# Kernel tuning notes

Measured on AMD Instinct MI355X. Metric: run time of the kernel, lower is better.

## Reference

```python
import jax, jax.numpy as jnp
import numpy as np

B, L, N, S, M = 4096, 512, 12, 128, 12


def setup_inputs() -> dict:
    key = jax.random.key(0)
    ks = jax.random.split(key, 8)
    sc = 1.0 / np.sqrt(S)
    scn = 1.0 / np.sqrt(N)
    return {
        "x": jax.random.normal(ks[0], (B, L, N), dtype=jnp.float32),
        "a0": jax.random.uniform(ks[1], (B, S), dtype=jnp.float32),
        "U_w": jax.random.uniform(ks[2], (N, S), minval=-scn, maxval=scn, dtype=jnp.float32),
        "U_b": jax.random.uniform(ks[3], (S,), minval=-scn, maxval=scn, dtype=jnp.float32),
        "W_w": jax.random.uniform(ks[4], (S, S), minval=-sc, maxval=sc, dtype=jnp.float32),
        "W_b": jax.random.uniform(ks[5], (S,), minval=-sc, maxval=sc, dtype=jnp.float32),
        "V_w": jax.random.uniform(ks[6], (S, M), minval=-sc, maxval=sc, dtype=jnp.float32),
        "V_b": jax.random.uniform(ks[7], (M,), minval=-sc, maxval=sc, dtype=jnp.float32),
    }


def reference(x, a0, U_w, U_b, W_w, W_b, V_w, V_b):
    # Elman RNN cell: a_t = relu(U(x_t) + W(a_{t-1})); output y = V(a_L)
    # Precompute input projection for all steps at once: [B,L,S]
    ux = jnp.einsum("bln,ns->bls", x, U_w) + U_b

    def step(a, ux_t):  # a: [B,S], ux_t: [B,S]
        a_new = jax.nn.relu(ux_t + a @ W_w + W_b)
        return a_new, None

    a_last, _ = jax.lax.scan(step, a0, jnp.swapaxes(ux, 0, 1))  # scan over L
    return a_last @ V_w + V_b  # [B, M]
```

## Files before the change

### kernel.cpp

```cpp
#include <hip/hip_runtime.h>
#include <hip/hip_bf16.h>

typedef __attribute__((ext_vector_type(8))) short bf16x8;
typedef __attribute__((ext_vector_type(4))) float f32x4;

#define L_SEQ 512
#define N_IN 12
#define S_DIM 128
#define M_OUT 12
#define LPAD 40
#define KT_STRIDE (16*LPAD)

__device__ inline short f2bf(float f) {
    union { float f; unsigned u; } q; q.f = f;
    unsigned r = (q.u + 0x7fffu + ((q.u >> 16) & 1u)) >> 16;
    return (short)r;
}
__device__ inline unsigned cvtpk(float lo, float hi) {
    unsigned r;
    asm("v_cvt_pk_bf16_f32 %0, %1, %2" : "=v"(r) : "v"(lo), "v"(hi));
    return r;
}
__device__ inline int s_perm(int kt, int q, int j) {
    return 32 * kt + 16 * (j >> 2) + 4 * q + (j & 3);
}
__device__ inline void block_sync() {
    asm volatile("s_waitcnt lgkmcnt(0)" ::: "memory");
    __builtin_amdgcn_s_barrier();
}

__global__ __launch_bounds__(256, 1)
void elman_kernel(const float* __restrict__ x,
                  const float* __restrict__ a0,
                  const float* __restrict__ U_w,
                  const float* __restrict__ U_b,
                  const float* __restrict__ W_w,
                  const float* __restrict__ W_b,
                  const float* __restrict__ V_w,
                  const float* __restrict__ V_b,
                  float* __restrict__ out)
{
    __shared__ __align__(16) short stx[2][4 * KT_STRIDE];

    const int tid  = threadIdx.x;
    const int w    = tid >> 6;
    const int l    = tid & 63;
    const int n    = l & 15;
    const int q    = l >> 4;
    const bool qodd = (q & 1);
    const int b0   = blockIdx.x * 16;
    const int row  = b0 + n;

    bf16x8 wf[2][4]; bf16x8 uf[2];
    #pragma unroll
    for (int h = 0; h < 2; ++h) {
        const int c = (2 * w + h) * 16 + n;
        #pragma unroll
        for (int li = 0; li < 4; ++li) {
            const int kt = (w + li) & 3;
            #pragma unroll
            for (int j = 0; j < 8; ++j)
                wf[h][li][j] = f2bf(W_w[(size_t)s_perm(kt, q, j) * S_DIM + c]);
        }
        #pragma unroll
        for (int j = 0; j < 8; ++j) {
            const int k = q * 8 + j;
            float v;
            if (k < N_IN)       v = U_w[(size_t)k * S_DIM + c];
            else if (k == N_IN) v = W_b[c] + U_b[c];
            else                v = 0.f;
            uf[h][j] = f2bf(v);
        }
    }

    for (int idx = tid; idx < 4 * 16 * 32; idx += 256) {
        const int kt = idx >> 9, r = (idx >> 5) & 15, qj = idx & 31;
        const int s = s_perm(kt, qj >> 3, qj & 7);
        stx[0][kt * KT_STRIDE + r * LPAD + qj] = f2bf(a0[(size_t)(b0 + r) * S_DIM + s]);
    }
    block_sync();

    const int fragoff = n * LPAD + q * 8;
    bf16x8 stOwn = *(const bf16x8*)&stx[0][((w + 0) & 3) * KT_STRIDE + fragoff];
    bf16x8 stf1  = *(const bf16x8*)&stx[0][((w + 1) & 3) * KT_STRIDE + fragoff];
    bf16x8 stf2  = *(const bf16x8*)&stx[0][((w + 2) & 3) * KT_STRIDE + fragoff];
    bf16x8 stf3  = *(const bf16x8*)&stx[0][((w + 3) & 3) * KT_STRIDE + fragoff];

    const float* xpA = x + (size_t)row * L_SEQ * N_IN + (q & 1) * 8;
    const float* xpB = xpA + (qodd ? 0 : 4);
    float4 xa0 = *(const float4*)(xpA + 0 * N_IN), xb0 = *(const float4*)(xpB + 0 * N_IN);
    float4 xa1 = *(const float4*)(xpA + 1 * N_IN), xb1 = *(const float4*)(xpB + 1 * N_IN);
    float4 xa2 = *(const float4*)(xpA + 2 * N_IN), xb2 = *(const float4*)(xpB + 2 * N_IN);
    float4 xa3 = *(const float4*)(xpA + 3 * N_IN), xb3 = *(const float4*)(xpB + 3 * N_IN);

#define MAKE_XF(XF, XA, XB) do {                                                       \
    union { unsigned u[4]; bf16x8 v; } xu_;                                            \
    xu_.u[0] = cvtpk(XA.x, XA.y);                                                      \
    xu_.u[1] = cvtpk(XA.z, XA.w);                                                      \
    xu_.u[2] = qodd ? 0x00003F80u : cvtpk(XB.x, XB.y);         \
    xu_.u[3] = qodd ? 0u          : cvtpk(XB.z, XB.w);                                 \
    XF = xu_.v;                                                                        \
} while (0)

    f32x4 accU0, accU1;
    {
        bf16x8 xf; MAKE_XF(xf, xa0, xb0);
        f32x4 z = {0.f, 0.f, 0.f, 0.f};
        accU0 = __builtin_amdgcn_mfma_f32_16x16x32_bf16(uf[0], xf, z, 0, 0, 0);
        accU1 = __builtin_amdgcn_mfma_f32_16x16x32_bf16(uf[1], xf, z, 0, 0, 0);
        xa0 = *(const float4*)(xpA + 4 * N_IN);
        xb0 = *(const float4*)(xpB + 4 * N_IN);
    }

#define STEP(XA, XB, TT, TNEXT) do {                                                   \
    f32x4 acc0, acc1;                                                                  \
    acc0 = __builtin_amdgcn_mfma_f32_16x16x32_bf16(wf[0][0], stOwn, accU0, 0, 0, 0);   \
    acc1 = __builtin_amdgcn_mfma_f32_16x16x32_bf16(wf[1][0], stOwn, accU1, 0, 0, 0);   \
    acc0 = __builtin_amdgcn_mfma_f32_16x16x32_bf16(wf[0][1], stf1, acc0, 0, 0, 0);     \
    acc1 = __builtin_amdgcn_mfma_f32_16x16x32_bf16(wf[1][1], stf1, acc1, 0, 0, 0);     \
    acc0 = __builtin_amdgcn_mfma_f32_16x16x32_bf16(wf[0][2], stf2, acc0, 0, 0, 0);     \
    acc1 = __builtin_amdgcn_mfma_f32_16x16x32_bf16(wf[1][2], stf2, acc1, 0, 0, 0);     \
    acc0 = __builtin_amdgcn_mfma_f32_16x16x32_bf16(wf[0][3], stf3, acc0, 0, 0, 0);     \
    acc1 = __builtin_amdgcn_mfma_f32_16x16x32_bf16(wf[1][3], stf3, acc1, 0, 0, 0);     \
                                  \
    {                                                                                  \
        bf16x8 xf_; MAKE_XF(xf_, XA, XB);                                              \
        const int tl_ = ((TNEXT) < L_SEQ) ? (TNEXT) : (L_SEQ - 1);                     \
        XA = *(const float4*)(xpA + (size_t)tl_ * N_IN);                               \
        XB = *(const float4*)(xpB + (size_t)tl_ * N_IN);                               \
        f32x4 z_ = {0.f, 0.f, 0.f, 0.f};                                               \
        accU0 = __builtin_amdgcn_mfma_f32_16x16x32_bf16(uf[0], xf_, z_, 0, 0, 0);      \
        accU1 = __builtin_amdgcn_mfma_f32_16x16x32_bf16(uf[1], xf_, z_, 0, 0, 0);      \
    }                                                                                  \
                   \
    {                                                                                  \
        union { unsigned u[4]; bf16x8 v; } su_;                                        \
        su_.u[0] = cvtpk(fmaxf(acc0[0], 0.f), fmaxf(acc0[1], 0.f));                    \
        su_.u[1] = cvtpk(fmaxf(acc0[2], 0.f), fmaxf(acc0[3], 0.f));                    \
        su_.u[2] = cvtpk(fmaxf(acc1[0], 0.f), fmaxf(acc1[1], 0.f));                    \
        su_.u[3] = cvtpk(fmaxf(acc1[2], 0.f), fmaxf(acc1[3], 0.f));                    \
        stOwn = su_.v;                                                                 \
    }                                                                                  \
    short* wr_ = &stx[(TT + 1) & 1][w * KT_STRIDE + fragoff];                          \
    *(bf16x8*)wr_ = stOwn;                                                             \
    block_sync();                                                                      \
    const short* rd_ = &stx[(TT + 1) & 1][0];                                          \
    stf1 = *(const bf16x8*)&rd_[((w + 1) & 3) * KT_STRIDE + fragoff];                  \
    stf2 = *(const bf16x8*)&rd_[((w + 2) & 3) * KT_STRIDE + fragoff];                  \
    stf3 = *(const bf16x8*)&rd_[((w + 3) & 3) * KT_STRIDE + fragoff];                  \
} while (0)

    for (int t = 0; t < L_SEQ; t += 4) {
        STEP(xa1, xb1, t + 0, t + 5);
        STEP(xa2, xb2, t + 1, t + 6);
        STEP(xa3, xb3, t + 2, t + 7);
        STEP(xa0, xb0, t + 3, t + 8);
    }
#undef STEP
#undef MAKE_XF

    if (w == 0) {
        f32x4 acc = {0.f, 0.f, 0.f, 0.f};
        #pragma unroll
        for (int li = 0; li < 4; ++li) {
            bf16x8 vf;
            #pragma unroll
            for (int j = 0; j < 8; ++j)
                vf[j] = (n < M_OUT)
                      ? f2bf(V_w[(size_t)s_perm(li, q, j) * M_OUT + n])
                      : (short)0;
            const bf16x8 stt = (li == 0) ? stOwn : (li == 1) ? stf1 : (li == 2) ? stf2 : stf3;
            acc = __builtin_amdgcn_mfma_f32_16x16x32_bf16(vf, stt, acc, 0, 0, 0);
        }
        #pragma unroll
        for (int j = 0; j < 4; ++j) {
            const int m = 4 * q + j;
            if (m < M_OUT)
                out[(size_t)row * M_OUT + m] = acc[j] + V_b[m];
        }
    }
}

extern "C" void kernel_launch(void* const* d_in, const int* in_sizes, int n_in,
                              void* d_out, int out_size, void* d_ws, size_t ws_size,
                              hipStream_t stream) {
    const float* x   = (const float*)d_in[0];
    const float* a0  = (const float*)d_in[1];
    const float* U_w = (const float*)d_in[2];
    const float* U_b = (const float*)d_in[3];
    const float* W_w = (const float*)d_in[4];
    const float* W_b = (const float*)d_in[5];
    const float* V_w = (const float*)d_in[6];
    const float* V_b = (const float*)d_in[7];
    float* out = (float*)d_out;

    hipLaunchKernelGGL(elman_kernel, dim3(4096 / 16), dim3(256), 0, stream,
                       x, a0, U_w, U_b, W_w, W_b, V_w, V_b, out);
}
```

Before: 135.7 us.

## Split recurrent matmul across eight waves with split-K accumulator chains

Doubles the block to 512 threads so each wave owns 16 hidden columns instead of 32. Each wave now issues four recurrent MFMAs per step, split into two independent accumulator chains that are summed before the ReLU. The goal is to shorten the serial MFMA dependency per timestep and put two waves on each SIMD to hide latency. In exchange, each wave writes a half-fragment to LDS and rereads all four state fragments every step, and the per-step barrier now spans eight waves.

```diff
diff --git a/kernel.cpp b/kernel.cpp
--- a/kernel.cpp
+++ b/kernel.cpp
@@ -3,6 +3,7 @@
 
 typedef __attribute__((ext_vector_type(8))) short bf16x8;
 typedef __attribute__((ext_vector_type(4))) float f32x4;
+typedef __attribute__((ext_vector_type(2))) unsigned uint2v;
 
 #define L_SEQ 512
 #define N_IN 12
@@ -29,7 +30,7 @@
     __builtin_amdgcn_s_barrier();
 }
 
-__global__ __launch_bounds__(256, 1)
+__global__ __launch_bounds__(512, 1)
 void elman_kernel(const float* __restrict__ x,
                   const float* __restrict__ a0,
                   const float* __restrict__ U_w,
@@ -51,29 +52,25 @@
     const int b0   = blockIdx.x * 16;
     const int row  = b0 + n;
 
-    bf16x8 wf[2][4]; bf16x8 uf[2];
-    #pragma unroll
-    for (int h = 0; h < 2; ++h) {
-        const int c = (2 * w + h) * 16 + n;
-        #pragma unroll
-        for (int li = 0; li < 4; ++li) {
-            const int kt = (w + li) & 3;
-            #pragma unroll
-            for (int j = 0; j < 8; ++j)
-                wf[h][li][j] = f2bf(W_w[(size_t)s_perm(kt, q, j) * S_DIM + c]);
-        }
+    const int c = w * 16 + n;
+    bf16x8 wf0, wf1, wf2, wf3; bf16x8 uf;
+    {
         #pragma unroll
         for (int j = 0; j < 8; ++j) {
+            wf0[j] = f2bf(W_w[(size_t)s_perm((w + 0) & 3, q, j) * S_DIM + c]);
+            wf1[j] = f2bf(W_w[(size_t)s_perm((w + 1) & 3, q, j) * S_DIM + c]);
+            wf2[j] = f2bf(W_w[(size_t)s_perm((w + 2) & 3, q, j) * S_DIM + c]);
+            wf3[j] = f2bf(W_w[(size_t)s_perm((w + 3) & 3, q, j) * S_DIM + c]);
             const int k = q * 8 + j;
             float v;
             if (k < N_IN)       v = U_w[(size_t)k * S_DIM + c];
             else if (k == N_IN) v = W_b[c] + U_b[c];
             else                v = 0.f;
-            uf[h][j] = f2bf(v);
+            uf[j] = f2bf(v);
         }
     }
 
-    for (int idx = tid; idx < 4 * 16 * 32; idx += 256) {
+    for (int idx = tid; idx < 4 * 16 * 32; idx += 512) {
         const int kt = idx >> 9, r = (idx >> 5) & 15, qj = idx & 31;
         const int s = s_perm(kt, qj >> 3, qj & 7);
         stx[0][kt * KT_STRIDE + r * LPAD + qj] = f2bf(a0[(size_t)(b0 + r) * S_DIM + s]);
@@ -81,10 +78,10 @@
     block_sync();
 
     const int fragoff = n * LPAD + q * 8;
-    bf16x8 stOwn = *(const bf16x8*)&stx[0][((w + 0) & 3) * KT_STRIDE + fragoff];
-    bf16x8 stf1  = *(const bf16x8*)&stx[0][((w + 1) & 3) * KT_STRIDE + fragoff];
-    bf16x8 stf2  = *(const bf16x8*)&stx[0][((w + 2) & 3) * KT_STRIDE + fragoff];
-    bf16x8 stf3  = *(const bf16x8*)&stx[0][((w + 3) & 3) * KT_STRIDE + fragoff];
+    bf16x8 stB0 = *(const bf16x8*)&stx[0][((w + 0) & 3) * KT_STRIDE + fragoff];
+    bf16x8 stB1 = *(const bf16x8*)&stx[0][((w + 1) & 3) * KT_STRIDE + fragoff];
+    bf16x8 stB2 = *(const bf16x8*)&stx[0][((w + 2) & 3) * KT_STRIDE + fragoff];
+    bf16x8 stB3 = *(const bf16x8*)&stx[0][((w + 3) & 3) * KT_STRIDE + fragoff];
 
     const float* xpA = x + (size_t)row * L_SEQ * N_IN + (q & 1) * 8;
     const float* xpB = xpA + (qodd ? 0 : 4);
@@ -102,52 +99,41 @@
     XF = xu_.v;                                                                        \
 } while (0)
 
-    f32x4 accU0, accU1;
+    f32x4 accU;
     {
         bf16x8 xf; MAKE_XF(xf, xa0, xb0);
         f32x4 z = {0.f, 0.f, 0.f, 0.f};
-        accU0 = __builtin_amdgcn_mfma_f32_16x16x32_bf16(uf[0], xf, z, 0, 0, 0);
-        accU1 = __builtin_amdgcn_mfma_f32_16x16x32_bf16(uf[1], xf, z, 0, 0, 0);
+        accU = __builtin_amdgcn_mfma_f32_16x16x32_bf16(uf, xf, z, 0, 0, 0);
         xa0 = *(const float4*)(xpA + 4 * N_IN);
         xb0 = *(const float4*)(xpB + 4 * N_IN);
     }
 
 #define STEP(XA, XB, TT, TNEXT) do {                                                   \
-    f32x4 acc0, acc1;                                                                  \
-    acc0 = __builtin_amdgcn_mfma_f32_16x16x32_bf16(wf[0][0], stOwn, accU0, 0, 0, 0);   \
-    acc1 = __builtin_amdgcn_mfma_f32_16x16x32_bf16(wf[1][0], stOwn, accU1, 0, 0, 0);   \
-    acc0 = __builtin_amdgcn_mfma_f32_16x16x32_bf16(wf[0][1], stf1, acc0, 0, 0, 0);     \
-    acc1 = __builtin_amdgcn_mfma_f32_16x16x32_bf16(wf[1][1], stf1, acc1, 0, 0, 0);     \
-    acc0 = __builtin_amdgcn_mfma_f32_16x16x32_bf16(wf[0][2], stf2, acc0, 0, 0, 0);     \
-    acc1 = __builtin_amdgcn_mfma_f32_16x16x32_bf16(wf[1][2], stf2, acc1, 0, 0, 0);     \
-    acc0 = __builtin_amdgcn_mfma_f32_16x16x32_bf16(wf[0][3], stf3, acc0, 0, 0, 0);     \
-    acc1 = __builtin_amdgcn_mfma_f32_16x16x32_bf16(wf[1][3], stf3, acc1, 0, 0, 0);     \
+                                \
+    f32x4 z_ = {0.f, 0.f, 0.f, 0.f};                                                   \
+    f32x4 acc_a = __builtin_amdgcn_mfma_f32_16x16x32_bf16(wf0, stB0, accU, 0, 0, 0);   \
+    f32x4 acc_b = __builtin_amdgcn_mfma_f32_16x16x32_bf16(wf2, stB2, z_,   0, 0, 0);   \
+    acc_a = __builtin_amdgcn_mfma_f32_16x16x32_bf16(wf1, stB1, acc_a, 0, 0, 0);        \
+    acc_b = __builtin_amdgcn_mfma_f32_16x16x32_bf16(wf3, stB3, acc_b, 0, 0, 0);        \
                                   \
     {                                                                                  \
         bf16x8 xf_; MAKE_XF(xf_, XA, XB);                                              \
         const int tl_ = ((TNEXT) < L_SEQ) ? (TNEXT) : (L_SEQ - 1);                     \
         XA = *(const float4*)(xpA + (size_t)tl_ * N_IN);                               \
         XB = *(const float4*)(xpB + (size_t)tl_ * N_IN);                               \
-        f32x4 z_ = {0.f, 0.f, 0.f, 0.f};                                               \
-        accU0 = __builtin_amdgcn_mfma_f32_16x16x32_bf16(uf[0], xf_, z_, 0, 0, 0);      \
-        accU1 = __builtin_amdgcn_mfma_f32_16x16x32_bf16(uf[1], xf_, z_, 0, 0, 0);      \
+        accU = __builtin_amdgcn_mfma_f32_16x16x32_bf16(uf, xf_, z_, 0, 0, 0);          \
     }                                                                                  \
-                   \
-    {                                                                                  \
-        union { unsigned u[4]; bf16x8 v; } su_;                                        \
-        su_.u[0] = cvtpk(fmaxf(acc0[0], 0.f), fmaxf(acc0[1], 0.f));                    \
-        su_.u[1] = cvtpk(fmaxf(acc0[2], 0.f), fmaxf(acc0[3], 0.f));                    \
-        su_.u[2] = cvtpk(fmaxf(acc1[0], 0.f), fmaxf(acc1[1], 0.f));                    \
-        su_.u[3] = cvtpk(fmaxf(acc1[2], 0.f), fmaxf(acc1[3], 0.f));                    \
-        stOwn = su_.v;                                                                 \
-    }                                                                                  \
-    short* wr_ = &stx[(TT + 1) & 1][w * KT_STRIDE + fragoff];                          \
-    *(bf16x8*)wr_ = stOwn;                                                             \
+               \
+    uint2v su_;                                                                        \
+    su_.x = cvtpk(fmaxf(acc_a[0] + acc_b[0], 0.f), fmaxf(acc_a[1] + acc_b[1], 0.f));   \
+    su_.y = cvtpk(fmaxf(acc_a[2] + acc_b[2], 0.f), fmaxf(acc_a[3] + acc_b[3], 0.f));   \
+    *(uint2v*)&stx[(TT + 1) & 1][(w >> 1) * KT_STRIDE + fragoff + (w & 1) * 4] = su_;  \
     block_sync();                                                                      \
     const short* rd_ = &stx[(TT + 1) & 1][0];                                          \
-    stf1 = *(const bf16x8*)&rd_[((w + 1) & 3) * KT_STRIDE + fragoff];                  \
-    stf2 = *(const bf16x8*)&rd_[((w + 2) & 3) * KT_STRIDE + fragoff];                  \
-    stf3 = *(const bf16x8*)&rd_[((w + 3) & 3) * KT_STRIDE + fragoff];                  \
+    stB0 = *(const bf16x8*)&rd_[((w + 0) & 3) * KT_STRIDE + fragoff];                  \
+    stB1 = *(const bf16x8*)&rd_[((w + 1) & 3) * KT_STRIDE + fragoff];                  \
+    stB2 = *(const bf16x8*)&rd_[((w + 2) & 3) * KT_STRIDE + fragoff];                  \
+    stB3 = *(const bf16x8*)&rd_[((w + 3) & 3) * KT_STRIDE + fragoff];                  \
 } while (0)
 
     for (int t = 0; t < L_SEQ; t += 4) {
@@ -169,7 +155,7 @@
                 vf[j] = (n < M_OUT)
                       ? f2bf(V_w[(size_t)s_perm(li, q, j) * M_OUT + n])
                       : (short)0;
-            const bf16x8 stt = (li == 0) ? stOwn : (li == 1) ? stf1 : (li == 2) ? stf2 : stf3;
+            const bf16x8 stt = (li == 0) ? stB0 : (li == 1) ? stB1 : (li == 2) ? stB2 : stB3;
             acc = __builtin_amdgcn_mfma_f32_16x16x32_bf16(vf, stt, acc, 0, 0, 0);
         }
         #pragma unroll
@@ -194,6 +180,6 @@
     const float* V_b = (const float*)d_in[7];
     float* out = (float*)d_out;
 
-    hipLaunchKernelGGL(elman_kernel, dim3(4096 / 16), dim3(256), 0, stream,
+    hipLaunchKernelGGL(elman_kernel, dim3(4096 / 16), dim3(512), 0, stream,
                        x, a0, U_w, U_b, W_w, W_b, V_w, V_b, out);
 }
```

After: 238.1 us. 75.5% more time.

## Add producer waves to stage x into LDS and split MFMA accumulation chains

Applied to the files above, without the earlier changes.

The block doubles to 512 threads. Four extra producer waves load and convert x from global memory into a 4-slot LDS ring two steps ahead, so the compute waves no longer issue global loads on the recurrence critical path. The compute waves also split the 8-MFMA dependent chain into two independent chains that are summed before the ReLU, which shortens per-step latency. In exchange, every step needs a barrier across eight waves instead of four.

```diff
diff --git a/kernel.cpp b/kernel.cpp
--- a/kernel.cpp
+++ b/kernel.cpp
@@ -29,7 +29,7 @@
     __builtin_amdgcn_s_barrier();
 }
 
-__global__ __launch_bounds__(256, 1)
+__global__ __launch_bounds__(512, 1)
 void elman_kernel(const float* __restrict__ x,
                   const float* __restrict__ a0,
                   const float* __restrict__ U_w,
@@ -41,6 +41,7 @@
                   float* __restrict__ out)
 {
     __shared__ __align__(16) short stx[2][4 * KT_STRIDE];
+    __shared__ __align__(16) short xr[4][64 * 8];
 
     const int tid  = threadIdx.x;
     const int w    = tid >> 6;
@@ -50,114 +51,122 @@
     const bool qodd = (q & 1);
     const int b0   = blockIdx.x * 16;
     const int row  = b0 + n;
+    const int fragoff = n * LPAD + q * 8;
+
+    const float* xpA = x + (size_t)row * L_SEQ * N_IN + (q & 1) * 8;
+    const float* xpB = xpA + (qodd ? 0 : 4);
+
+#define MAKE_XF(XF, XA, XB) do {                                                       \
+    union { unsigned uu[4]; bf16x8 v; } xu_;                                           \
+    xu_.uu[0] = cvtpk(XA.x, XA.y);                                                     \
+    xu_.uu[1] = cvtpk(XA.z, XA.w);                                                     \
+    xu_.uu[2] = qodd ? 0x00003F80u : cvtpk(XB.x, XB.y);        \
+    xu_.uu[3] = qodd ? 0u          : cvtpk(XB.z, XB.w);                                \
+    XF = xu_.v;                                                                        \
+} while (0)
 
     bf16x8 wf[2][4]; bf16x8 uf[2];
-    #pragma unroll
-    for (int h = 0; h < 2; ++h) {
-        const int c = (2 * w + h) * 16 + n;
-        #pragma unroll
-        for (int li = 0; li < 4; ++li) {
-            const int kt = (w + li) & 3;
+    if (w < 4) {
+        #pragma unroll
+        for (int h = 0; h < 2; ++h) {
+            const int c = (2 * w + h) * 16 + n;
             #pragma unroll
-            for (int j = 0; j < 8; ++j)
-                wf[h][li][j] = f2bf(W_w[(size_t)s_perm(kt, q, j) * S_DIM + c]);
-        }
-        #pragma unroll
-        for (int j = 0; j < 8; ++j) {
-            const int k = q * 8 + j;
-            float v;
-            if (k < N_IN)       v = U_w[(size_t)k * S_DIM + c];
-            else if (k == N_IN) v = W_b[c] + U_b[c];
-            else                v = 0.f;
-            uf[h][j] = f2bf(v);
-        }
-    }
-
-    for (int idx = tid; idx < 4 * 16 * 32; idx += 256) {
+            for (int li = 0; li < 4; ++li) {
+                const int kt = (w + li) & 3;
+                #pragma unroll
+                for (int j = 0; j < 8; ++j)
+                    wf[h][li][j] = f2bf(W_w[(size_t)s_perm(kt, q, j) * S_DIM + c]);
+            }
+            #pragma unroll
+            for (int j = 0; j < 8; ++j) {
+                const int k = q * 8 + j;
+                float v;
+                if (k < N_IN)       v = U_w[(size_t)k * S_DIM + c];
+                else if (k == N_IN) v = W_b[c] + U_b[c];
+                else                v = 0.f;
+                uf[h][j] = f2bf(v);
+            }
+        }
+    }
+
+    for (int idx = tid; idx < 4 * 16 * 32; idx += 512) {
         const int kt = idx >> 9, r = (idx >> 5) & 15, qj = idx & 31;
         const int s = s_perm(kt, qj >> 3, qj & 7);
         stx[0][kt * KT_STRIDE + r * LPAD + qj] = f2bf(a0[(size_t)(b0 + r) * S_DIM + s]);
     }
+
+    float4 xa, xb;
+    if (w >= 4) {
+        const int h = w & 3;
+        if (h < 2) {
+            float4 pa = *(const float4*)(xpA + (size_t)h * N_IN);
+            float4 pb = *(const float4*)(xpB + (size_t)h * N_IN);
+            bf16x8 xf; MAKE_XF(xf, pa, pb);
+            *(bf16x8*)&xr[h][l * 8] = xf;
+        }
+        const int sf = ((h + 2) & 3) + 2;
+        xa = *(const float4*)(xpA + (size_t)sf * N_IN);
+        xb = *(const float4*)(xpB + (size_t)sf * N_IN);
+    }
     block_sync();
 
-    const int fragoff = n * LPAD + q * 8;
-    bf16x8 stOwn = *(const bf16x8*)&stx[0][((w + 0) & 3) * KT_STRIDE + fragoff];
-    bf16x8 stf1  = *(const bf16x8*)&stx[0][((w + 1) & 3) * KT_STRIDE + fragoff];
-    bf16x8 stf2  = *(const bf16x8*)&stx[0][((w + 2) & 3) * KT_STRIDE + fragoff];
-    bf16x8 stf3  = *(const bf16x8*)&stx[0][((w + 3) & 3) * KT_STRIDE + fragoff];
-
-    const float* xpA = x + (size_t)row * L_SEQ * N_IN + (q & 1) * 8;
-    const float* xpB = xpA + (qodd ? 0 : 4);
-    float4 xa0 = *(const float4*)(xpA + 0 * N_IN), xb0 = *(const float4*)(xpB + 0 * N_IN);
-    float4 xa1 = *(const float4*)(xpA + 1 * N_IN), xb1 = *(const float4*)(xpB + 1 * N_IN);
-    float4 xa2 = *(const float4*)(xpA + 2 * N_IN), xb2 = *(const float4*)(xpB + 2 * N_IN);
-    float4 xa3 = *(const float4*)(xpA + 3 * N_IN), xb3 = *(const float4*)(xpB + 3 * N_IN);
-
-#define MAKE_XF(XF, XA, XB) do {                                                       \
-    union { unsigned u[4]; bf16x8 v; } xu_;                                            \
-    xu_.u[0] = cvtpk(XA.x, XA.y);                                                      \
-    xu_.u[1] = cvtpk(XA.z, XA.w);                                                      \
-    xu_.u[2] = qodd ? 0x00003F80u : cvtpk(XB.x, XB.y);         \
-    xu_.u[3] = qodd ? 0u          : cvtpk(XB.z, XB.w);                                 \
-    XF = xu_.v;                                                                        \
-} while (0)
-
+    bf16x8 stOwn, stf1, stf2, stf3, xfc;
     f32x4 accU0, accU1;
-    {
-        bf16x8 xf; MAKE_XF(xf, xa0, xb0);
+    if (w < 4) {
+        const short* rd = &stx[0][0];
+        stOwn = *(const bf16x8*)&rd[((w + 0) & 3) * KT_STRIDE + fragoff];
+        stf1  = *(const bf16x8*)&rd[((w + 1) & 3) * KT_STRIDE + fragoff];
+        stf2  = *(const bf16x8*)&rd[((w + 2) & 3) * KT_STRIDE + fragoff];
+        stf3  = *(const bf16x8*)&rd[((w + 3) & 3) * KT_STRIDE + fragoff];
+        bf16x8 xf0 = *(const bf16x8*)&xr[0][l * 8];
+        xfc        = *(const bf16x8*)&xr[1][l * 8];
         f32x4 z = {0.f, 0.f, 0.f, 0.f};
-        accU0 = __builtin_amdgcn_mfma_f32_16x16x32_bf16(uf[0], xf, z, 0, 0, 0);
-        accU1 = __builtin_amdgcn_mfma_f32_16x16x32_bf16(uf[1], xf, z, 0, 0, 0);
-        xa0 = *(const float4*)(xpA + 4 * N_IN);
-        xb0 = *(const float4*)(xpB + 4 * N_IN);
-    }
-
-#define STEP(XA, XB, TT, TNEXT) do {                                                   \
-    f32x4 acc0, acc1;                                                                  \
-    acc0 = __builtin_amdgcn_mfma_f32_16x16x32_bf16(wf[0][0], stOwn, accU0, 0, 0, 0);   \
-    acc1 = __builtin_amdgcn_mfma_f32_16x16x32_bf16(wf[1][0], stOwn, accU1, 0, 0, 0);   \
-    acc0 = __builtin_amdgcn_mfma_f32_16x16x32_bf16(wf[0][1], stf1, acc0, 0, 0, 0);     \
-    acc1 = __builtin_amdgcn_mfma_f32_16x16x32_bf16(wf[1][1], stf1, acc1, 0, 0, 0);     \
-    acc0 = __builtin_amdgcn_mfma_f32_16x16x32_bf16(wf[0][2], stf2, acc0, 0, 0, 0);     \
-    acc1 = __builtin_amdgcn_mfma_f32_16x16x32_bf16(wf[1][2], stf2, acc1, 0, 0, 0);     \
-    acc0 = __builtin_amdgcn_mfma_f32_16x16x32_bf16(wf[0][3], stf3, acc0, 0, 0, 0);     \
-    acc1 = __builtin_amdgcn_mfma_f32_16x16x32_bf16(wf[1][3], stf3, acc1, 0, 0, 0);     \
-                                  \
-    {                                                                                  \
-        bf16x8 xf_; MAKE_XF(xf_, XA, XB);                                              \
-        const int tl_ = ((TNEXT) < L_SEQ) ? (TNEXT) : (L_SEQ - 1);                     \
-        XA = *(const float4*)(xpA + (size_t)tl_ * N_IN);                               \
-        XB = *(const float4*)(xpB + (size_t)tl_ * N_IN);                               \
-        f32x4 z_ = {0.f, 0.f, 0.f, 0.f};                                               \
-        accU0 = __builtin_amdgcn_mfma_f32_16x16x32_bf16(uf[0], xf_, z_, 0, 0, 0);      \
-        accU1 = __builtin_amdgcn_mfma_f32_16x16x32_bf16(uf[1], xf_, z_, 0, 0, 0);      \
-    }                                                                                  \
-                   \
-    {                                                                                  \
-        union { unsigned u[4]; bf16x8 v; } su_;                                        \
-        su_.u[0] = cvtpk(fmaxf(acc0[0], 0.f), fmaxf(acc0[1], 0.f));                    \
-        su_.u[1] = cvtpk(fmaxf(acc0[2], 0.f), fmaxf(acc0[3], 0.f));                    \
-        su_.u[2] = cvtpk(fmaxf(acc1[0], 0.f), fmaxf(acc1[1], 0.f));                    \
-        su_.u[3] = cvtpk(fmaxf(acc1[2], 0.f), fmaxf(acc1[3], 0.f));                    \
-        stOwn = su_.v;                                                                 \
-    }                                                                                  \
-    short* wr_ = &stx[(TT + 1) & 1][w * KT_STRIDE + fragoff];                          \
-    *(bf16x8*)wr_ = stOwn;                                                             \
-    block_sync();                                                                      \
-    const short* rd_ = &stx[(TT + 1) & 1][0];                                          \
-    stf1 = *(const bf16x8*)&rd_[((w + 1) & 3) * KT_STRIDE + fragoff];                  \
-    stf2 = *(const bf16x8*)&rd_[((w + 2) & 3) * KT_STRIDE + fragoff];                  \
-    stf3 = *(const bf16x8*)&rd_[((w + 3) & 3) * KT_STRIDE + fragoff];                  \
-} while (0)
+        accU0 = __builtin_amdgcn_mfma_f32_16x16x32_bf16(uf[0], xf0, z, 0, 0, 0);
+        accU1 = __builtin_amdgcn_mfma_f32_16x16x32_bf16(uf[1], xf0, z, 0, 0, 0);
+    }
 
     for (int t = 0; t < L_SEQ; t += 4) {
-        STEP(xa1, xb1, t + 0, t + 5);
-        STEP(xa2, xb2, t + 1, t + 6);
-        STEP(xa3, xb3, t + 2, t + 7);
-        STEP(xa0, xb0, t + 3, t + 8);
-    }
-#undef STEP
-#undef MAKE_XF
+        #pragma unroll
+        for (int u = 0; u < 4; ++u) {
+            const int tt = t + u;
+            if (w < 4) {
+                f32x4 z = {0.f, 0.f, 0.f, 0.f};
+                f32x4 c0a = __builtin_amdgcn_mfma_f32_16x16x32_bf16(wf[0][0], stOwn, accU0, 0, 0, 0);
+                f32x4 c1a = __builtin_amdgcn_mfma_f32_16x16x32_bf16(wf[1][0], stOwn, accU1, 0, 0, 0);
+                accU0 = __builtin_amdgcn_mfma_f32_16x16x32_bf16(uf[0], xfc, z, 0, 0, 0);
+                accU1 = __builtin_amdgcn_mfma_f32_16x16x32_bf16(uf[1], xfc, z, 0, 0, 0);
+                c0a = __builtin_amdgcn_mfma_f32_16x16x32_bf16(wf[0][1], stf1, c0a, 0, 0, 0);
+                c1a = __builtin_amdgcn_mfma_f32_16x16x32_bf16(wf[1][1], stf1, c1a, 0, 0, 0);
+                f32x4 c0b = __builtin_amdgcn_mfma_f32_16x16x32_bf16(wf[0][2], stf2, z, 0, 0, 0);
+                f32x4 c1b = __builtin_amdgcn_mfma_f32_16x16x32_bf16(wf[1][2], stf2, z, 0, 0, 0);
+                c0b = __builtin_amdgcn_mfma_f32_16x16x32_bf16(wf[0][3], stf3, c0b, 0, 0, 0);
+                c1b = __builtin_amdgcn_mfma_f32_16x16x32_bf16(wf[1][3], stf3, c1b, 0, 0, 0);
+                union { unsigned uu[4]; bf16x8 v; } su;
+                su.uu[0] = cvtpk(fmaxf(c0a[0] + c0b[0], 0.f), fmaxf(c0a[1] + c0b[1], 0.f));
+                su.uu[1] = cvtpk(fmaxf(c0a[2] + c0b[2], 0.f), fmaxf(c0a[3] + c0b[3], 0.f));
+                su.uu[2] = cvtpk(fmaxf(c1a[0] + c1b[0], 0.f), fmaxf(c1a[1] + c1b[1], 0.f));
+                su.uu[3] = cvtpk(fmaxf(c1a[2] + c1b[2], 0.f), fmaxf(c1a[3] + c1b[3], 0.f));
+                stOwn = su.v;
+                *(bf16x8*)&stx[(tt + 1) & 1][w * KT_STRIDE + fragoff] = stOwn;
+            } else {
+                if ((w & 3) == ((u + 2) & 3)) {
+                    bf16x8 xf; MAKE_XF(xf, xa, xb);
+                    *(bf16x8*)&xr[(tt + 2) & 3][l * 8] = xf;
+                    const int s2 = (tt + 6 < L_SEQ) ? (tt + 6) : (L_SEQ - 1);
+                    xa = *(const float4*)(xpA + (size_t)s2 * N_IN);
+                    xb = *(const float4*)(xpB + (size_t)s2 * N_IN);
+                }
+            }
+            block_sync();
+            if (w < 4) {
+                const short* rd = &stx[(tt + 1) & 1][0];
+                stf1 = *(const bf16x8*)&rd[((w + 1) & 3) * KT_STRIDE + fragoff];
+                stf2 = *(const bf16x8*)&rd[((w + 2) & 3) * KT_STRIDE + fragoff];
+                stf3 = *(const bf16x8*)&rd[((w + 3) & 3) * KT_STRIDE + fragoff];
+                xfc  = *(const bf16x8*)&xr[(tt + 2) & 3][l * 8];
+            }
+        }
+    }
 
     if (w == 0) {
         f32x4 acc = {0.f, 0.f, 0.f, 0.f};
@@ -179,6 +188,7 @@
                 out[(size_t)row * M_OUT + m] = acc[j] + V_b[m];
         }
     }
+#undef MAKE_XF
 }
 
 extern "C" void kernel_launch(void* const* d_in, const int* in_sizes, int n_in,
@@ -194,6 +204,6 @@
     const float* V_b = (const float*)d_in[7];
     float* out = (float*)d_out;
 
-    hipLaunchKernelGGL(elman_kernel, dim3(4096 / 16), dim3(256), 0, stream,
+    hipLaunchKernelGGL(elman_kernel, dim3(4096 / 16), dim3(512), 0, stream,
                        x, a0, U_w, U_b, W_w, W_b, V_w, V_b, out);
 }
```

Result: faster. 122.1 us (-10.0%).

## Split recurrent MFMA chain into two accumulators and deepen x prefetch pipeline

Applied to the files above, without the earlier changes.

Restructures the per-step recurrence so the four dependent K-tile MFMAs are split into two independent accumulation chains (tiles 0-1 and 2-3) summed before the ReLU. This shortens the serial MFMA dependency latency on the critical path. The shared-memory reads of the other waves' state fragments move to the start of each step, so the barrier sits at the end. The input-projection MFMAs for the next step are interleaved into the chain, and x loads are prefetched one step further ahead. The cost is more live registers and extra adds per step, and the final output stage now reloads fragments from shared memory.

```diff
diff --git a/kernel.cpp b/kernel.cpp
--- a/kernel.cpp
+++ b/kernel.cpp
@@ -50,17 +50,30 @@
     const bool qodd = (q & 1);
     const int b0   = blockIdx.x * 16;
     const int row  = b0 + n;
+    const int fragoff = n * LPAD + q * 8;
+
+    const float* xpA = x + (size_t)row * L_SEQ * N_IN + (q & 1) * 8;
+    const float* xpB = xpA + (qodd ? 0 : 4);
+
+#define MAKE_XF(XF, XA, XB) do {                                                       \
+    union { unsigned uu[4]; bf16x8 v; } xu_;                                           \
+    xu_.uu[0] = cvtpk(XA.x, XA.y);                                                     \
+    xu_.uu[1] = cvtpk(XA.z, XA.w);                                                     \
+    xu_.uu[2] = qodd ? 0x00003F80u : cvtpk(XB.x, XB.y);        \
+    xu_.uu[3] = qodd ? 0u          : cvtpk(XB.z, XB.w);                                \
+    XF = xu_.v;                                                                        \
+} while (0)
 
     bf16x8 wf[2][4]; bf16x8 uf[2];
     #pragma unroll
-    for (int h = 0; h < 2; ++h) {
-        const int c = (2 * w + h) * 16 + n;
+    for (int hh = 0; hh < 2; ++hh) {
+        const int c = (2 * w + hh) * 16 + n;
         #pragma unroll
         for (int li = 0; li < 4; ++li) {
             const int kt = (w + li) & 3;
             #pragma unroll
             for (int j = 0; j < 8; ++j)
-                wf[h][li][j] = f2bf(W_w[(size_t)s_perm(kt, q, j) * S_DIM + c]);
+                wf[hh][li][j] = f2bf(W_w[(size_t)s_perm(kt, q, j) * S_DIM + c]);
         }
         #pragma unroll
         for (int j = 0; j < 8; ++j) {
@@ -69,7 +82,7 @@
             if (k < N_IN)       v = U_w[(size_t)k * S_DIM + c];
             else if (k == N_IN) v = W_b[c] + U_b[c];
             else                v = 0.f;
-            uf[h][j] = f2bf(v);
+            uf[hh][j] = f2bf(v);
         }
     }
 
@@ -78,88 +91,80 @@
         const int s = s_perm(kt, qj >> 3, qj & 7);
         stx[0][kt * KT_STRIDE + r * LPAD + qj] = f2bf(a0[(size_t)(b0 + r) * S_DIM + s]);
     }
-    block_sync();
-
-    const int fragoff = n * LPAD + q * 8;
-    bf16x8 stOwn = *(const bf16x8*)&stx[0][((w + 0) & 3) * KT_STRIDE + fragoff];
-    bf16x8 stf1  = *(const bf16x8*)&stx[0][((w + 1) & 3) * KT_STRIDE + fragoff];
-    bf16x8 stf2  = *(const bf16x8*)&stx[0][((w + 2) & 3) * KT_STRIDE + fragoff];
-    bf16x8 stf3  = *(const bf16x8*)&stx[0][((w + 3) & 3) * KT_STRIDE + fragoff];
-
-    const float* xpA = x + (size_t)row * L_SEQ * N_IN + (q & 1) * 8;
-    const float* xpB = xpA + (qodd ? 0 : 4);
-    float4 xa0 = *(const float4*)(xpA + 0 * N_IN), xb0 = *(const float4*)(xpB + 0 * N_IN);
-    float4 xa1 = *(const float4*)(xpA + 1 * N_IN), xb1 = *(const float4*)(xpB + 1 * N_IN);
+
+    float4 t0A = *(const float4*)(xpA + 0 * N_IN), t0B = *(const float4*)(xpB + 0 * N_IN);
+    float4 t1A = *(const float4*)(xpA + 1 * N_IN), t1B = *(const float4*)(xpB + 1 * N_IN);
     float4 xa2 = *(const float4*)(xpA + 2 * N_IN), xb2 = *(const float4*)(xpB + 2 * N_IN);
     float4 xa3 = *(const float4*)(xpA + 3 * N_IN), xb3 = *(const float4*)(xpB + 3 * N_IN);
-
-#define MAKE_XF(XF, XA, XB) do {                                                       \
-    union { unsigned u[4]; bf16x8 v; } xu_;                                            \
-    xu_.u[0] = cvtpk(XA.x, XA.y);                                                      \
-    xu_.u[1] = cvtpk(XA.z, XA.w);                                                      \
-    xu_.u[2] = qodd ? 0x00003F80u : cvtpk(XB.x, XB.y);         \
-    xu_.u[3] = qodd ? 0u          : cvtpk(XB.z, XB.w);                                 \
-    XF = xu_.v;                                                                        \
-} while (0)
-
+    float4 xa0 = *(const float4*)(xpA + 4 * N_IN), xb0 = *(const float4*)(xpB + 4 * N_IN);
+    float4 xa1 = *(const float4*)(xpA + 5 * N_IN), xb1 = *(const float4*)(xpB + 5 * N_IN);
+
+    bf16x8 xfc;
     f32x4 accU0, accU1;
     {
-        bf16x8 xf; MAKE_XF(xf, xa0, xb0);
+        bf16x8 xf0; MAKE_XF(xf0, t0A, t0B);
         f32x4 z = {0.f, 0.f, 0.f, 0.f};
-        accU0 = __builtin_amdgcn_mfma_f32_16x16x32_bf16(uf[0], xf, z, 0, 0, 0);
-        accU1 = __builtin_amdgcn_mfma_f32_16x16x32_bf16(uf[1], xf, z, 0, 0, 0);
-        xa0 = *(const float4*)(xpA + 4 * N_IN);
-        xb0 = *(const float4*)(xpB + 4 * N_IN);
-    }
-
-#define STEP(XA, XB, TT, TNEXT) do {                                                   \
-    f32x4 acc0, acc1;                                                                  \
-    acc0 = __builtin_amdgcn_mfma_f32_16x16x32_bf16(wf[0][0], stOwn, accU0, 0, 0, 0);   \
-    acc1 = __builtin_amdgcn_mfma_f32_16x16x32_bf16(wf[1][0], stOwn, accU1, 0, 0, 0);   \
-    acc0 = __builtin_amdgcn_mfma_f32_16x16x32_bf16(wf[0][1], stf1, acc0, 0, 0, 0);     \
-    acc1 = __builtin_amdgcn_mfma_f32_16x16x32_bf16(wf[1][1], stf1, acc1, 0, 0, 0);     \
-    acc0 = __builtin_amdgcn_mfma_f32_16x16x32_bf16(wf[0][2], stf2, acc0, 0, 0, 0);     \
-    acc1 = __builtin_amdgcn_mfma_f32_16x16x32_bf16(wf[1][2], stf2, acc1, 0, 0, 0);     \
-    acc0 = __builtin_amdgcn_mfma_f32_16x16x32_bf16(wf[0][3], stf3, acc0, 0, 0, 0);     \
-    acc1 = __builtin_amdgcn_mfma_f32_16x16x32_bf16(wf[1][3], stf3, acc1, 0, 0, 0);     \
-                                  \
-    {                                                                                  \
-        bf16x8 xf_; MAKE_XF(xf_, XA, XB);                                              \
-        const int tl_ = ((TNEXT) < L_SEQ) ? (TNEXT) : (L_SEQ - 1);                     \
-        XA = *(const float4*)(xpA + (size_t)tl_ * N_IN);                               \
-        XB = *(const float4*)(xpB + (size_t)tl_ * N_IN);                               \
-        f32x4 z_ = {0.f, 0.f, 0.f, 0.f};                                               \
-        accU0 = __builtin_amdgcn_mfma_f32_16x16x32_bf16(uf[0], xf_, z_, 0, 0, 0);      \
-        accU1 = __builtin_amdgcn_mfma_f32_16x16x32_bf16(uf[1], xf_, z_, 0, 0, 0);      \
-    }                                                                                  \
-                   \
-    {                                                                                  \
-        union { unsigned u[4]; bf16x8 v; } su_;                                        \
-        su_.u[0] = cvtpk(fmaxf(acc0[0], 0.f), fmaxf(acc0[1], 0.f));                    \
-        su_.u[1] = cvtpk(fmaxf(acc0[2], 0.f), fmaxf(acc0[3], 0.f));                    \
-        su_.u[2] = cvtpk(fmaxf(acc1[0], 0.f), fmaxf(acc1[1], 0.f));                    \
-        su_.u[3] = cvtpk(fmaxf(acc1[2], 0.f), fmaxf(acc1[3], 0.f));                    \
-        stOwn = su_.v;                                                                 \
-    }                                                                                  \
-    short* wr_ = &stx[(TT + 1) & 1][w * KT_STRIDE + fragoff];                          \
-    *(bf16x8*)wr_ = stOwn;                                                             \
-    block_sync();                                                                      \
-    const short* rd_ = &stx[(TT + 1) & 1][0];                                          \
+        accU0 = __builtin_amdgcn_mfma_f32_16x16x32_bf16(uf[0], xf0, z, 0, 0, 0);
+        accU1 = __builtin_amdgcn_mfma_f32_16x16x32_bf16(uf[1], xf0, z, 0, 0, 0);
+        MAKE_XF(xfc, t1A, t1B);
+    }
+    block_sync();
+
+    bf16x8 stOwn = *(const bf16x8*)&stx[0][((w + 0) & 3) * KT_STRIDE + fragoff];
+    bf16x8 stf1, stf2, stf3;
+
+#define BODY(XA, XB, UU) do {                                                          \
+    const int tt = t + (UU);                                                           \
+    const short* rd_ = &stx[tt & 1][0];                                                \
     stf1 = *(const bf16x8*)&rd_[((w + 1) & 3) * KT_STRIDE + fragoff];                  \
     stf2 = *(const bf16x8*)&rd_[((w + 2) & 3) * KT_STRIDE + fragoff];                  \
     stf3 = *(const bf16x8*)&rd_[((w + 3) & 3) * KT_STRIDE + fragoff];                  \
+    f32x4 z_ = {0.f, 0.f, 0.f, 0.f};                                                   \
+                             \
+    f32x4 c0a = __builtin_amdgcn_mfma_f32_16x16x32_bf16(wf[0][0], stOwn, accU0, 0, 0, 0); \
+    f32x4 c1a = __builtin_amdgcn_mfma_f32_16x16x32_bf16(wf[1][0], stOwn, accU1, 0, 0, 0); \
+    f32x4 nU0 = __builtin_amdgcn_mfma_f32_16x16x32_bf16(uf[0], xfc, z_, 0, 0, 0);      \
+    f32x4 nU1 = __builtin_amdgcn_mfma_f32_16x16x32_bf16(uf[1], xfc, z_, 0, 0, 0);      \
+                                                                    \
+    c0a = __builtin_amdgcn_mfma_f32_16x16x32_bf16(wf[0][1], stf1, c0a, 0, 0, 0);       \
+    c1a = __builtin_amdgcn_mfma_f32_16x16x32_bf16(wf[1][1], stf1, c1a, 0, 0, 0);       \
+    f32x4 c0b = __builtin_amdgcn_mfma_f32_16x16x32_bf16(wf[0][2], stf2, z_, 0, 0, 0);  \
+    f32x4 c1b = __builtin_amdgcn_mfma_f32_16x16x32_bf16(wf[1][2], stf2, z_, 0, 0, 0);  \
+    c0b = __builtin_amdgcn_mfma_f32_16x16x32_bf16(wf[0][3], stf3, c0b, 0, 0, 0);       \
+    c1b = __builtin_amdgcn_mfma_f32_16x16x32_bf16(wf[1][3], stf3, c1b, 0, 0, 0);       \
+                            \
+    MAKE_XF(xfc, XA, XB);                                                              \
+    {                                                                                  \
+        const int s2_ = (tt + 6 < L_SEQ) ? (tt + 6) : (L_SEQ - 1);                     \
+        XA = *(const float4*)(xpA + (size_t)s2_ * N_IN);                               \
+        XB = *(const float4*)(xpB + (size_t)s2_ * N_IN);                               \
+    }                                                                                  \
+    accU0 = nU0; accU1 = nU1;                                                          \
+                                           \
+    union { unsigned uu[4]; bf16x8 v; } su;                                            \
+    su.uu[0] = cvtpk(fmaxf(c0a[0] + c0b[0], 0.f), fmaxf(c0a[1] + c0b[1], 0.f));        \
+    su.uu[1] = cvtpk(fmaxf(c0a[2] + c0b[2], 0.f), fmaxf(c0a[3] + c0b[3], 0.f));        \
+    su.uu[2] = cvtpk(fmaxf(c1a[0] + c1b[0], 0.f), fmaxf(c1a[1] + c1b[1], 0.f));        \
+    su.uu[3] = cvtpk(fmaxf(c1a[2] + c1b[2], 0.f), fmaxf(c1a[3] + c1b[3], 0.f));        \
+    stOwn = su.v;                                                                      \
+    *(bf16x8*)&stx[(tt + 1) & 1][w * KT_STRIDE + fragoff] = stOwn;                     \
+    block_sync();                                                                      \
 } while (0)
 
     for (int t = 0; t < L_SEQ; t += 4) {
-        STEP(xa1, xb1, t + 0, t + 5);
-        STEP(xa2, xb2, t + 1, t + 6);
-        STEP(xa3, xb3, t + 2, t + 7);
-        STEP(xa0, xb0, t + 3, t + 8);
-    }
-#undef STEP
+        BODY(xa2, xb2, 0);
+        BODY(xa3, xb3, 1);
+        BODY(xa0, xb0, 2);
+        BODY(xa1, xb1, 3);
+    }
+#undef BODY
 #undef MAKE_XF
 
     if (w == 0) {
+        const short* rd = &stx[0][0];
+        stf1 = *(const bf16x8*)&rd[1 * KT_STRIDE + fragoff];
+        stf2 = *(const bf16x8*)&rd[2 * KT_STRIDE + fragoff];
+        stf3 = *(const bf16x8*)&rd[3 * KT_STRIDE + fragoff];
         f32x4 acc = {0.f, 0.f, 0.f, 0.f};
         #pragma unroll
         for (int li = 0; li < 4; ++li) {
```

Result: slower. 146.0 us (+7.6%).
